# Kernel tuning notes

Hardware: AMD Instinct MI355X
Metric: run time of the kernel (lower is better)

## Reference

```python
import jax, jax.numpy as jnp
import numpy as np

N = 20000      # number of nodes (softmax vocab)
H = 40         # LSTM hidden size (generator_layers[-1])
DW = 128       # W_down_generator_size
ND = 16        # noise_dim
RW = 8         # rw_len
NS = 512       # n_sample
EPS = 1e-20
TAU = 1.0


def setup_inputs() -> dict:
    key = jax.random.key(0)
    ks = jax.random.split(key, 12)
    f32 = jnp.float32
    def rn(k, shape, scale):
        return jax.random.normal(k, shape, dtype=f32) * scale
    s_h = 1.0 / np.sqrt(H)
    s_n = 1.0 / np.sqrt(N)
    s_d = 1.0 / np.sqrt(DW)
    return {
        "z": jax.random.normal(ks[0], (NS, ND), dtype=f32),
        "gumbel_u": jax.random.uniform(ks[1], (RW, NS, N), dtype=f32),
        "l1_w": rn(ks[2], (ND, H), 1.0 / np.sqrt(ND)),
        "l1_b": jnp.zeros((H,), f32),
        "l2_w": rn(ks[3], (H, H), s_h),
        "l2_b": jnp.zeros((H,), f32),
        "l3_w": rn(ks[4], (H, H), s_h),
        "l3_b": jnp.zeros((H,), f32),
        "w_ih": rn(ks[5], (DW, 4 * H), s_h),
        "w_hh": rn(ks[6], (H, 4 * H), s_h),
        "b_ih": jnp.zeros((4 * H,), f32),
        "b_hh": jnp.zeros((4 * H,), f32),
        "W_up": rn(ks[7], (H, N), s_n),
        "b_up": rn(ks[8], (N,), s_n),
        "W_down": rn(ks[9], (N, DW), s_d),
        "n_sample": NS,
    }


def reference(z, gumbel_u, l1_w, l1_b, l2_w, l2_b, l3_w, l3_b,
              w_ih, w_hh, b_ih, b_hh, W_up, b_up, W_down, n_sample):
    # initial LSTM state from noise (single generator layer)
    inter = jnp.tanh(z @ l1_w + l1_b)             # [NS, H]
    h0 = jnp.tanh(inter @ l2_w + l2_b)            # [NS, H]
    c0 = jnp.tanh(inter @ l3_w + l3_b)            # [NS, H]
    x0 = jnp.zeros((n_sample, W_down.shape[1]), dtype=z.dtype)  # [NS, DW]

    def lstm_cell(x, h, c):
        g = x @ w_ih + b_ih + h @ w_hh + b_hh      # [NS, 4H]
        i, f, gg, o = jnp.split(g, 4, axis=-1)      # PyTorch gate order i,f,g,o
        c2 = jax.nn.sigmoid(f) * c + jax.nn.sigmoid(i) * jnp.tanh(gg)
        h2 = jax.nn.sigmoid(o) * jnp.tanh(c2)
        return h2, c2

    def step(carry, u):
        x, h, c = carry
        h, c = lstm_cell(x, h, c)
        logits = h @ W_up + b_up                   # [NS, N]
        gnoise = -jnp.log(-jnp.log(u + EPS) + EPS) # Gumbel(0,1)
        y = jax.nn.softmax((logits + gnoise) / TAU, axis=1)
        # hard (straight-through) sample
        y_hard = jax.nn.one_hot(jnp.argmax(y, axis=-1), y.shape[-1], dtype=y.dtype)
        y = jax.lax.stop_gradient(y_hard - y) + y
        x = y @ W_down                             # [NS, DW]
        return (x, h, c), y

    _, outs = jax.lax.scan(step, (x0, h0, c0), gumbel_u)  # [RW, NS, N]
    return jnp.transpose(outs, (1, 0, 2))                 # [NS, RW, N]
```

## Files before the change

kernel.cpp:

```cpp
#include <hip/hip_runtime.h>
#include <math.h>

#define KN    20000
#define KH    40
#define KDW   128
#define KND   16
#define KRW   8
#define KNS   512
#define KCH   79
#define NROW  (KRW*KNS)
#define CMAX  32
#define KEPS  1e-20f
#define KLN2  0.69314718055994531f
#define HBND  6.32455532f
#define NINF  (-__builtin_inff())

typedef float floatx4 __attribute__((ext_vector_type(4)));

__device__ __forceinline__ float sigmoidf_(float x) { return 1.0f / (1.0f + expf(-x)); }

__device__ __forceinline__ unsigned long long packsc_(float v, int col) {
  unsigned u = __float_as_uint(v);
  unsigned key = (u >> 31) ? ~u : (u | 0x80000000u);
  return ((unsigned long long)key << 32) | (unsigned)(~col);
}
__device__ __forceinline__ float gumbel_(float u) {
  float t = fmaf(-KLN2, __log2f(u + KEPS), KEPS);
  return -KLN2 * __log2f(t);
}

__global__ void __launch_bounds__(256) k_init_wnorm(
    const float* __restrict__ z,
    const float* __restrict__ l1w, const float* __restrict__ l1b,
    const float* __restrict__ l2w, const float* __restrict__ l2b,
    const float* __restrict__ l3w, const float* __restrict__ l3b,
    const float* __restrict__ b_ih, const float* __restrict__ b_hh,
    const float* __restrict__ w_hh, const float* __restrict__ W_up,
    const float* __restrict__ b_up,
    float* __restrict__ h, float* __restrict__ c,
    float* __restrict__ wpart, float* __restrict__ bpart) {
  int tid = threadIdx.x;
  __shared__ float zs[KND], inter[KH], h0[KH], c0[KH], g[4*KH];
  __shared__ float wm[4], bm[4];
  if (blockIdx.x >= KNS) {
    int b = blockIdx.x - KNS;
    int j = b*256 + tid;
    int lane = tid & 63, grp = tid >> 6;
    float ss = 0.f, ab = 0.f;
    if (j < KN) {
#pragma unroll
      for (int k = 0; k < KH; ++k) { float w = W_up[k*KN + j]; ss = fmaf(w, w, ss); }
      ab = fabsf(b_up[j]);
    }
    float wn = sqrtf(ss);
#pragma unroll
    for (int d = 32; d > 0; d >>= 1) {
      wn = fmaxf(wn, __shfl_xor(wn, d, 64));
      ab = fmaxf(ab, __shfl_xor(ab, d, 64));
    }
    if (lane == 0) { wm[grp] = wn; bm[grp] = ab; }
    __syncthreads();
    if (tid == 0) {
      wpart[b] = fmaxf(fmaxf(wm[0], wm[1]), fmaxf(wm[2], wm[3]));
      bpart[b] = fmaxf(fmaxf(bm[0], bm[1]), fmaxf(bm[2], bm[3]));
    }
    return;
  }
  int s = blockIdx.x;
  if (tid < KND) zs[tid] = z[s*KND + tid];
  __syncthreads();
  if (tid < KH) {
    float a = l1b[tid];
#pragma unroll
    for (int k = 0; k < KND; ++k) a = fmaf(zs[k], l1w[k*KH + tid], a);
    inter[tid] = tanhf(a);
  }
  __syncthreads();
  if (tid < KH) {
    float a2 = l2b[tid], a3 = l3b[tid];
#pragma unroll
    for (int k = 0; k < KH; ++k) {
      float iv = inter[k];
      a2 = fmaf(iv, l2w[k*KH + tid], a2);
      a3 = fmaf(iv, l3w[k*KH + tid], a3);
    }
    h0[tid] = tanhf(a2);
    c0[tid] = tanhf(a3);
  }
  __syncthreads();
  if (tid < 4*KH) {
    float a = b_ih[tid] + b_hh[tid];
#pragma unroll 8
    for (int k = 0; k < KH; ++k) a = fmaf(h0[k], w_hh[k*4*KH + tid], a);
    g[tid] = a;
  }
  __syncthreads();
  if (tid < KH) {
    float gi = g[tid], gf = g[KH+tid], gg = g[2*KH+tid], go = g[3*KH+tid];
    float cn = sigmoidf_(gf) * c0[tid] + sigmoidf_(gi) * tanhf(gg);
    float hn = sigmoidf_(go) * tanhf(cn);
    h[s*KH + tid] = hn;
    c[s*KH + tid] = cn;
  }
}

__global__ void __launch_bounds__(256) k_score_zero(
    const float* __restrict__ gu,
    float* __restrict__ pp,
    float* __restrict__ out) {
  int s = blockIdx.x, t = blockIdx.y;
  int tid = threadIdx.x, grp = tid >> 6, lane = tid & 63;
  __shared__ float cm[KCH + 1];
  const float* urow = gu + ((size_t)t*KNS + s)*KN;
  float* orow = out + ((size_t)s*KRW + t)*KN;

  floatx4 u4[20];
#pragma unroll
  for (int it = 0; it < 20; ++it) {
    int col = (it*256 + tid) * 4;
    u4[it] = *(const floatx4*)(urow + (col < KN ? col : KN - 4));
  }
  float m[20];
#pragma unroll
  for (int it = 0; it < 20; ++it) {
    int col = (it*256 + tid) * 4;
    bool v = col < KN;
    float mm = fmaxf(fmaxf(u4[it][0], u4[it][1]), fmaxf(u4[it][2], u4[it][3]));
    m[it] = v ? mm : NINF;
  }
#pragma unroll
  for (int d = 32; d > 0; d >>= 1) {
#pragma unroll
    for (int it = 0; it < 20; ++it)
      m[it] = fmaxf(m[it], __shfl_xor(m[it], d, 64));
  }
#pragma unroll
  for (int it = 0; it < 20; ++it) {
    int ch = it*4 + grp;
    if (lane == 0 && ch < KCH) cm[ch] = m[it];
  }
  __syncthreads();
  if (tid < KCH) pp[((size_t)s*KRW + t)*KCH + tid] = cm[tid];

  floatx4 zv = (floatx4)(0.f);
#pragma unroll
  for (int it = 0; it < 20; ++it) {
    int col = (it*256 + tid) * 4;
    if (col < KN) __builtin_nontemporal_store(zv, (floatx4*)(orow + col));
  }
}

__global__ void __launch_bounds__(128) k_cands(
    const float* __restrict__ pp,
    const float* __restrict__ gu,
    const float* __restrict__ b_up,
    const float* __restrict__ wpart,
    const float* __restrict__ bpart,
    int2* __restrict__ candbuf,
    int* __restrict__ candcnt) {
  int r = blockIdx.x;
  int s = r / KRW, t = r - s*KRW;
  int tid = threadIdx.x, lane = tid & 63, wave = tid >> 6;
  __shared__ float sThr, sBm;
  __shared__ int chlist[KCH], nch, ncand, ovf;
  if (tid == 0) { nch = 0; ncand = 0; ovf = 0; }
  __syncthreads();

  if (wave == 0) {
    float ua = pp[(size_t)r*KCH + lane];
    float ub = (lane + 64 < KCH) ? pp[(size_t)r*KCH + lane + 64] : NINF;
    float um = fmaxf(ua, ub);
    float wa = (lane < KCH) ? wpart[lane] : NINF;
    float wb = (lane + 64 < KCH) ? wpart[lane + 64] : NINF;
    float wm = fmaxf(wa, wb);
    float ba = (lane < KCH) ? bpart[lane] : NINF;
    float bb = (lane + 64 < KCH) ? bpart[lane + 64] : NINF;
    float bmx = fmaxf(ba, bb);
#pragma unroll
    for (int d = 32; d > 0; d >>= 1) {
      um  = fmaxf(um,  __shfl_xor(um,  d, 64));
      wm  = fmaxf(wm,  __shfl_xor(wm,  d, 64));
      bmx = fmaxf(bmx, __shfl_xor(bmx, d, 64));
    }
    if (lane == 0) {
      float lb = gumbel_(um) - bmx;
      sThr = lb - (2.0f * HBND * wm * 1.001f + 1e-3f) - 2e-3f;
      sBm  = bmx;
    }
  }
  __syncthreads();
  float thr = sThr, bmx = sBm;
  if (tid < KCH && gumbel_(pp[(size_t)r*KCH + tid]) + bmx + 2e-3f >= thr) {
    int i = atomicAdd(&nch, 1);
    chlist[i] = tid;
  }
  __syncthreads();
  int nchunks = nch;
  const float* urow = gu + ((size_t)t*KNS + s)*KN;
  for (int ci = 0; ci < nchunks; ++ci) {
    int base = chlist[ci]*256;
#pragma unroll
    for (int half = 0; half < 2; ++half) {
      int col = base + half*128 + tid;
      if (col < KN) {
        float key = gumbel_(urow[col]) + b_up[col];
        if (key >= thr) {
          int i = atomicAdd(&ncand, 1);
          if (i < CMAX) candbuf[(size_t)r*CMAX + i] = make_int2(__float_as_int(key), col);
          else ovf = 1;
        }
      }
    }
  }
  __syncthreads();
  if (tid == 0) candcnt[r] = ovf ? -1 : ncand;
}

__global__ void __launch_bounds__(256) k_final(
    const int2* __restrict__ candbuf, const int* __restrict__ candcnt,
    const float* __restrict__ gu,
    const float* __restrict__ W_up, const float* __restrict__ b_up,
    const float* __restrict__ hg, const float* __restrict__ cg,
    const float* __restrict__ W_down,
    const float* __restrict__ w_ih, const float* __restrict__ w_hh,
    const float* __restrict__ b_ih, const float* __restrict__ b_hh,
    float* __restrict__ out) {
  int s = blockIdx.x, tid = threadIdx.x;
  int wave = tid >> 6, lane = tid & 63;
  __shared__ float hs[KH], cs[KH], xs[KDW], g[4*KH];
  __shared__ unsigned long long wbest[4];
  __shared__ int widxS;

  if (tid < KH) { hs[tid] = hg[s*KH + tid]; cs[tid] = cg[s*KH + tid]; }
  __syncthreads();

  for (int t = 0; t < KRW; ++t) {
    int r = s*KRW + t;
    int nc = candcnt[r];
    unsigned long long best = 0ull;
    if (nc >= 0) {
      for (int ci = wave; ci < nc; ci += 4) {
        int2 cd = candbuf[(size_t)r*CMAX + ci];
        float key = __int_as_float(cd.x);
        int col = cd.y;
        float p = (lane < KH) ? hs[lane] * W_up[lane*KN + col] : 0.f;
#pragma unroll
        for (int d = 32; d > 0; d >>= 1) p += __shfl_xor(p, d, 64);
        unsigned long long pk = packsc_(key + p, col);
        if (pk > best) best = pk;
      }
    } else {
      const float* urow = gu + ((size_t)t*KNS + s)*KN;
      for (int col = tid; col < KN; col += 256) {
        float sc = gumbel_(urow[col]) + b_up[col];
#pragma unroll
        for (int k = 0; k < KH; ++k) sc = fmaf(hs[k], W_up[k*KN + col], sc);
        unsigned long long pk = packsc_(sc, col);
        if (pk > best) best = pk;
      }
    }
#pragma unroll
    for (int d = 32; d > 0; d >>= 1) {
      unsigned long long q = (unsigned long long)__shfl_xor((long long)best, d, 64);
      if (q > best) best = q;
    }
    if (lane == 0) wbest[wave] = best;
    __syncthreads();
    if (tid == 0) {
      unsigned long long fb = wbest[0];
      if (wbest[1] > fb) fb = wbest[1];
      if (wbest[2] > fb) fb = wbest[2];
      if (wbest[3] > fb) fb = wbest[3];
      int w = (int)(~(unsigned)(fb & 0xFFFFFFFFull));
      widxS = w;
      out[((size_t)s*KRW + t)*KN + w] = 1.0f;
    }
    __syncthreads();
    if (t < KRW - 1) {
      if (tid < KDW) xs[tid] = W_down[(size_t)widxS*KDW + tid];
      __syncthreads();
      if (tid < 4*KH) {
        float a = b_ih[tid] + b_hh[tid];
#pragma unroll 8
        for (int k = 0; k < KDW; ++k) a = fmaf(xs[k], w_ih[k*4*KH + tid], a);
#pragma unroll 8
        for (int k = 0; k < KH; ++k) a = fmaf(hs[k], w_hh[k*4*KH + tid], a);
        g[tid] = a;
      }
      __syncthreads();
      if (tid < KH) {
        float gi = g[tid], gf = g[KH+tid], gg2 = g[2*KH+tid], go = g[3*KH+tid];
        float cn = sigmoidf_(gf) * cs[tid] + sigmoidf_(gi) * tanhf(gg2);
        float hn_ = sigmoidf_(go) * tanhf(cn);
        hs[tid] = hn_; cs[tid] = cn;
      }
      __syncthreads();
    }
  }
}

extern "C" void kernel_launch(void* const* d_in, const int* in_sizes, int n_in,
                              void* d_out, int out_size, void* d_ws, size_t ws_size,
                              hipStream_t stream) {
  const float* z      = (const float*)d_in[0];
  const float* gu     = (const float*)d_in[1];
  const float* l1w    = (const float*)d_in[2];
  const float* l1b    = (const float*)d_in[3];
  const float* l2w    = (const float*)d_in[4];
  const float* l2b    = (const float*)d_in[5];
  const float* l3w    = (const float*)d_in[6];
  const float* l3b    = (const float*)d_in[7];
  const float* w_ih   = (const float*)d_in[8];
  const float* w_hh   = (const float*)d_in[9];
  const float* b_ih   = (const float*)d_in[10];
  const float* b_hh   = (const float*)d_in[11];
  const float* W_up   = (const float*)d_in[12];
  const float* b_up   = (const float*)d_in[13];
  const float* W_down = (const float*)d_in[14];
  float* out = (float*)d_out;

  char* ws = (char*)d_ws;
  size_t off = 0;
  float* h  = (float*)(ws + off); off += (size_t)KNS*KH*4;
  float* c  = (float*)(ws + off); off += (size_t)KNS*KH*4;
  float* pp = (float*)(ws + off); off += (size_t)NROW*KCH*4;
  float* wpart = (float*)(ws + off); off += 128*4;
  float* bpart = (float*)(ws + off); off += 128*4;
  int2* candbuf = (int2*)(ws + off); off += (size_t)NROW*CMAX*8;
  int* candcnt = (int*)(ws + off);

  k_init_wnorm<<<KNS + KCH, 256, 0, stream>>>(z, l1w, l1b, l2w, l2b, l3w, l3b,
                                              b_ih, b_hh, w_hh, W_up, b_up,
                                              h, c, wpart, bpart);

  k_score_zero<<<dim3(KNS, KRW), 256, 0, stream>>>(gu, pp, out);

  k_cands<<<NROW, 128, 0, stream>>>(pp, gu, b_up, wpart, bpart, candbuf, candcnt);

  k_final<<<KNS, 256, 0, stream>>>(candbuf, candcnt, gu, W_up, b_up, h, c,
                                   W_down, w_ih, w_hh, b_ih, b_hh, out);
}
```

Before: 190.6 us.

## Stream gumbel rows into LDS via global_load_lds in 1024-thread score kernel

The score/zero kernel now uses 1024 threads per block and loads each row of uniform noise straight into shared memory with direct global-to-LDS loads, instead of holding 20 float4 values per thread in registers. The zero-fill stores of the output row are issued before the loads so writes and reads can overlap. Per-chunk maxima are then computed from LDS with fewer reduction passes per thread. The cost is about 80KB of LDS per block, which limits blocks per CU and may reduce latency hiding.

```diff
diff --git a/kernel.cpp b/kernel.cpp
--- a/kernel.cpp
+++ b/kernel.cpp
@@ -16,6 +16,8 @@
 #define NINF  (-__builtin_inff())
 
 typedef float floatx4 __attribute__((ext_vector_type(4)));
+#define AS1 __attribute__((address_space(1)))
+#define AS3 __attribute__((address_space(3)))
 
 __device__ __forceinline__ float sigmoidf_(float x) { return 1.0f / (1.0f + expf(-x)); }
 
@@ -104,50 +106,64 @@
   }
 }
 
-__global__ void __launch_bounds__(256) k_score_zero(
+__global__ void __launch_bounds__(1024) k_score_zero(
     const float* __restrict__ gu,
     float* __restrict__ pp,
     float* __restrict__ out) {
   int s = blockIdx.x, t = blockIdx.y;
-  int tid = threadIdx.x, grp = tid >> 6, lane = tid & 63;
-  __shared__ float cm[KCH + 1];
+  int tid = threadIdx.x, wave = tid >> 6, lane = tid & 63;
+  extern __shared__ float smem[];
+  float* lds = smem;
+  float* cm  = smem + KN;
   const float* urow = gu + ((size_t)t*KNS + s)*KN;
   float* orow = out + ((size_t)s*KRW + t)*KN;
 
-  floatx4 u4[20];
-#pragma unroll
-  for (int it = 0; it < 20; ++it) {
-    int col = (it*256 + tid) * 4;
-    u4[it] = *(const floatx4*)(urow + (col < KN ? col : KN - 4));
-  }
-  float m[20];
-#pragma unroll
-  for (int it = 0; it < 20; ++it) {
-    int col = (it*256 + tid) * 4;
-    bool v = col < KN;
-    float mm = fmaxf(fmaxf(u4[it][0], u4[it][1]), fmaxf(u4[it][2], u4[it][3]));
-    m[it] = v ? mm : NINF;
+  floatx4 zv = (floatx4)(0.f);
+#pragma unroll
+  for (int k = 0; k < 5; ++k) {
+    int i = k*1024 + tid;
+    if (i < 5000) __builtin_nontemporal_store(zv, (floatx4*)orow + i);
+  }
+
+#pragma unroll
+  for (int k = 0; k < 5; ++k) {
+    int i = k*1024 + tid;
+    if (i < 5000) {
+      const AS1 unsigned* gsrc =
+          (const AS1 unsigned*)(urow + (size_t)i*4);
+      AS3 unsigned* ldst =
+          (AS3 unsigned*)(lds + (size_t)(k*1024 + wave*64)*4);
+      __builtin_amdgcn_global_load_lds(gsrc, ldst, 16, 0, 0);
+    }
+  }
+  __syncthreads();
+
+  float m[5];
+#pragma unroll
+  for (int k = 0; k < 5; ++k) {
+    int i = k*1024 + tid;
+    bool v = i < 5000;
+    floatx4 u4;
+    if (v) u4 = *(const floatx4*)(lds + (size_t)i*4);
+    else   u4 = (floatx4)(0.f);
+    float mm = fmaxf(fmaxf(u4[0], u4[1]), fmaxf(u4[2], u4[3]));
+    m[k] = v ? mm : NINF;
   }
 #pragma unroll
   for (int d = 32; d > 0; d >>= 1) {
 #pragma unroll
-    for (int it = 0; it < 20; ++it)
-      m[it] = fmaxf(m[it], __shfl_xor(m[it], d, 64));
-  }
-#pragma unroll
-  for (int it = 0; it < 20; ++it) {
-    int ch = it*4 + grp;
-    if (lane == 0 && ch < KCH) cm[ch] = m[it];
+    for (int k = 0; k < 5; ++k)
+      m[k] = fmaxf(m[k], __shfl_xor(m[k], d, 64));
+  }
+  if (lane == 0) {
+#pragma unroll
+    for (int k = 0; k < 5; ++k) {
+      int ch = k*16 + wave;
+      if (ch < KCH) cm[ch] = m[k];
+    }
   }
   __syncthreads();
   if (tid < KCH) pp[((size_t)s*KRW + t)*KCH + tid] = cm[tid];
-
-  floatx4 zv = (floatx4)(0.f);
-#pragma unroll
-  for (int it = 0; it < 20; ++it) {
-    int col = (it*256 + tid) * 4;
-    if (col < KN) __builtin_nontemporal_store(zv, (floatx4*)(orow + col));
-  }
 }
 
 __global__ void __launch_bounds__(128) k_cands(
@@ -333,7 +349,7 @@
                                               b_ih, b_hh, w_hh, W_up, b_up,
                                               h, c, wpart, bpart);
 
-  k_score_zero<<<dim3(KNS, KRW), 256, 0, stream>>>(gu, pp, out);
+  k_score_zero<<<dim3(KNS, KRW), 1024, (size_t)(KN + 128)*4, stream>>>(gu, pp, out);
 
   k_cands<<<NROW, 128, 0, stream>>>(pp, gu, b_up, wpart, bpart, candbuf, candcnt);
 
```

Measured after the change: 187.5 us. About the same (-1.6%).
